# Optimization experiments

Hardware: AMD Instinct MI355X
Metric: run time of the kernel (lower is better)

## Reference

```python
import jax, jax.numpy as jnp
import numpy as np

L, B, T, C, H, V = 4, 4, 1024, 1024, 16, 32000
DH = C // H
FF = 4 * C
IGNORE = 5
EPS = 1e-5


def setup_inputs() -> dict:
    key = jax.random.key(0)
    ks = jax.random.split(key, 12)
    s = 0.02
    return {
        "idx": jax.random.randint(ks[0], (B, T), 0, V),
        "targets": jax.random.randint(ks[1], (B, T), 0, V),
        "tok_emb": jax.random.normal(ks[2], (V, C), jnp.float32) * s,
        "pos_emb": jax.random.normal(ks[3], (T, C), jnp.float32) * s,
        "Wq": jax.random.normal(ks[4], (L, C, C), jnp.float32) * s,
        "Wk": jax.random.normal(ks[5], (L, C, C), jnp.float32) * s,
        "Wv": jax.random.normal(ks[6], (L, C, C), jnp.float32) * s,
        "Wo": jax.random.normal(ks[7], (L, C, C), jnp.float32) * s,
        "bo": jnp.zeros((L, C), jnp.float32),
        "ln1_g": jnp.ones((L, C), jnp.float32),
        "ln1_b": jnp.zeros((L, C), jnp.float32),
        "ln2_g": jnp.ones((L, C), jnp.float32),
        "ln2_b": jnp.zeros((L, C), jnp.float32),
        "W1": jax.random.normal(ks[8], (L, C, FF), jnp.float32) * s,
        "b1": jnp.zeros((L, FF), jnp.float32),
        "W2": jax.random.normal(ks[9], (L, FF, C), jnp.float32) * s,
        "b2": jnp.zeros((L, C), jnp.float32),
        "lnf_g": jnp.ones((C,), jnp.float32),
        "lnf_b": jnp.zeros((C,), jnp.float32),
        "Whead": jax.random.normal(ks[10], (C, V), jnp.float32) * s,
        "bhead": jnp.zeros((V,), jnp.float32),
    }


def _layernorm(x, g, b):
    mu = jnp.mean(x, axis=-1, keepdims=True)
    var = jnp.var(x, axis=-1, keepdims=True)
    return (x - mu) * jax.lax.rsqrt(var + EPS) * g + b


def _gpt_forward(idx, targets, tok_emb, pos_emb, Wq, Wk, Wv, Wo, bo,
                 ln1_g, ln1_b, ln2_g, ln2_b, W1, b1, W2, b2,
                 lnf_g, lnf_b, Whead, bhead):
    x = tok_emb[idx] + pos_emb[None, :, :]  # [B,T,C]
    causal = jnp.tril(jnp.ones((T, T), bool))
    for i in range(L):
        h = _layernorm(x, ln1_g[i], ln1_b[i])
        q = (h @ Wq[i]).reshape(B, T, H, DH)
        k = (h @ Wk[i]).reshape(B, T, H, DH)
        v = (h @ Wv[i]).reshape(B, T, H, DH)
        wei = jnp.einsum("bqhd,bkhd->bhqk", q, k) * (DH ** -0.5)
        wei = jnp.where(causal[None, None], wei, -jnp.inf)
        wei = jax.nn.softmax(wei, axis=-1)
        att = jnp.einsum("bhqk,bkhd->bqhd", wei, v).reshape(B, T, C)
        x = x + att @ Wo[i] + bo[i]
        h = _layernorm(x, ln2_g[i], ln2_b[i])
        x = x + jax.nn.gelu(h @ W1[i] + b1[i], approximate=False) @ W2[i] + b2[i]
    x = _layernorm(x, lnf_g, lnf_b)
    logits = x @ Whead + bhead  # [B,T,V]
    # cross-entropy with ignore_index=5
    lg = logits.reshape(B * T, V)
    tg = targets.reshape(B * T)
    logp = jax.nn.log_softmax(lg, axis=-1)
    nll = -jnp.take_along_axis(logp, tg[:, None], axis=-1)[:, 0]
    valid = (tg != IGNORE).astype(lg.dtype)
    loss = jnp.sum(nll * valid) / jnp.maximum(jnp.sum(valid), 1.0)
    return logits, loss


def reference(idx, targets, tok_emb, pos_emb, Wq, Wk, Wv, Wo, bo,
              ln1_g, ln1_b, ln2_g, ln2_b, W1, b1, W2, b2,
              lnf_g, lnf_b, Whead, bhead):
    return _gpt_forward(idx, targets, tok_emb, pos_emb, Wq, Wk, Wv, Wo, bo,
                        ln1_g, ln1_b, ln2_g, ln2_b, W1, b1, W2, b2,
                        lnf_g, lnf_b, Whead, bhead)
```

## Files before the change

kernel.cpp:

```cpp
#include <hip/hip_runtime.h>
#include <cstdint>
#include <cstddef>

#define Lx 4
#define Bx 4
#define Tx 1024
#define Cx 1024
#define Hx 16
#define DHx 64
#define FFx 4096
#define Vx 32000
#define BTx 4096

typedef __attribute__((ext_vector_type(8))) __bf16 bf16x8;
typedef __attribute__((ext_vector_type(4))) float f32x4;
typedef __attribute__((ext_vector_type(8))) short short8;

__device__ __forceinline__ float bflo(unsigned u){ return __builtin_bit_cast(float, u << 16); }
__device__ __forceinline__ float bfhi(unsigned u){ return __builtin_bit_cast(float, u & 0xffff0000u); }
__device__ __forceinline__ float bf2f(short s){ return bflo((unsigned)(unsigned short)s); }
__device__ __forceinline__ short f2bf(float f){
  unsigned u = __builtin_bit_cast(unsigned, f);
  u += 0x7fffu + ((u >> 16) & 1u);
  return (short)(u >> 16);
}

__device__ __forceinline__ void gload_lds16(const short* g, short* l){
  __builtin_amdgcn_global_load_lds(
      (const __attribute__((address_space(1))) unsigned int*)g,
      (__attribute__((address_space(3))) unsigned int*)l, 16, 0, 0);
}

__device__ __forceinline__ int xcd_swizzle(int orig, int nwg){
  const int q = nwg >> 3, r = nwg & 7;
  const int xcd = orig & 7, wg = orig >> 3;
  const int base = (xcd < r) ? xcd * (q + 1) : r * (q + 1) + (xcd - r) * q;
  return base + wg;
}

__global__ __launch_bounds__(256) void embed_kernel(
    const int* __restrict__ idx, const float* __restrict__ tok,
    const float* __restrict__ pos, float* __restrict__ x)
{
  const int bt = blockIdx.x;
  const int t  = bt & (Tx - 1);
  const int tid = threadIdx.x;
  const int tk = idx[bt];
  float4 a = *(const float4*)&tok[((size_t)tk << 10) + (tid << 2)];
  const float4 p = *(const float4*)&pos[((size_t)t << 10) + (tid << 2)];
  a.x += p.x; a.y += p.y; a.z += p.z; a.w += p.w;
  *(float4*)&x[((size_t)bt << 10) + (tid << 2)] = a;
}

__global__ __launch_bounds__(256) void ln_kernel(
    const float* __restrict__ x, const float* __restrict__ g,
    const float* __restrict__ b, short* __restrict__ out)
{
  const int row = blockIdx.x;
  const int tid = threadIdx.x;
  const float4 v = *(const float4*)&x[((size_t)row << 10) + (tid << 2)];
  float s  = v.x + v.y + v.z + v.w;
  float ss = v.x*v.x + v.y*v.y + v.z*v.z + v.w*v.w;
  #pragma unroll
  for (int off = 32; off >= 1; off >>= 1) {
    s  += __shfl_down(s, off);
    ss += __shfl_down(ss, off);
  }
  __shared__ float rs[4], rss[4];
  const int lane = tid & 63, w = tid >> 6;
  if (lane == 0) { rs[w] = s; rss[w] = ss; }
  __syncthreads();
  s  = rs[0] + rs[1] + rs[2] + rs[3];
  ss = rss[0] + rss[1] + rss[2] + rss[3];
  const float mu  = s * (1.0f / Cx);
  const float var = ss * (1.0f / Cx) - mu * mu;
  const float rstd = rsqrtf(var + 1e-5f);
  const float4 g4 = *(const float4*)&g[tid << 2];
  const float4 b4 = *(const float4*)&b[tid << 2];
  short4 o;
  o.x = f2bf((v.x - mu) * rstd * g4.x + b4.x);
  o.y = f2bf((v.y - mu) * rstd * g4.y + b4.y);
  o.z = f2bf((v.z - mu) * rstd * g4.z + b4.z);
  o.w = f2bf((v.w - mu) * rstd * g4.w + b4.w);
  *(short4*)&out[((size_t)row << 10) + (tid << 2)] = o;
}

__global__ __launch_bounds__(256) void wconv_kernel(
    const float* __restrict__ W, short* __restrict__ Wt, int K, int N)
{
  __shared__ float tile[32][33];
  const int n0 = blockIdx.x << 5, k0 = blockIdx.y << 5;
  const int tx = threadIdx.x & 31, ty = threadIdx.x >> 5;
  #pragma unroll
  for (int r = 0; r < 4; ++r)
    tile[ty + (r << 3)][tx] = __builtin_nontemporal_load(
        &W[(size_t)(k0 + ty + (r << 3)) * N + n0 + tx]);
  __syncthreads();
  #pragma unroll
  for (int r = 0; r < 4; ++r)
    Wt[(size_t)(n0 + ty + (r << 3)) * K + k0 + tx] = f2bf(tile[tx][ty + (r << 3)]);
}

__global__ __launch_bounds__(256) void wconv4_kernel(
    const float* __restrict__ Wq, const float* __restrict__ Wk,
    const float* __restrict__ Wv, const float* __restrict__ Wo,
    short* __restrict__ qkvT, short* __restrict__ woT)
{
  __shared__ float tile[32][33];
  const int z = blockIdx.z;
  const float* W = (z == 0) ? Wq : (z == 1) ? Wk : (z == 2) ? Wv : Wo;
  short* Wt = (z < 3) ? qkvT + (size_t)z * Cx * Cx : woT;
  const int n0 = blockIdx.x << 5, k0 = blockIdx.y << 5;
  const int tx = threadIdx.x & 31, ty = threadIdx.x >> 5;
  #pragma unroll
  for (int r = 0; r < 4; ++r)
    tile[ty + (r << 3)][tx] = __builtin_nontemporal_load(
        &W[(size_t)(k0 + ty + (r << 3)) * Cx + n0 + tx]);
  __syncthreads();
  #pragma unroll
  for (int r = 0; r < 4; ++r)
    Wt[(size_t)(n0 + ty + (r << 3)) * Cx + k0 + tx] = f2bf(tile[tx][ty + (r << 3)]);
}

template<int MODE>
__global__ __launch_bounds__(256) void gemm_kernel(
    const short* __restrict__ A, const short* __restrict__ Bt,
    const float* __restrict__ bias, const float* __restrict__ res,
    float* __restrict__ outF, short* __restrict__ outB, int N, int K)
{
  __shared__ __align__(16) short sA[128 * 32];
  __shared__ __align__(16) short sB[128 * 32];
  const int tid  = threadIdx.x;
  const int lane = tid & 63;
  const int wave = tid >> 6;
  const int bid  = xcd_swizzle((int)blockIdx.x, (int)gridDim.x);
  const int tm = (bid & 31) << 7;
  const int tn = (bid >> 5) << 7;
  const int wm = ((wave >> 1) & 1) << 6;
  const int wn = (wave & 1) << 6;

  f32x4 acc[4][4] = {};

  const int o1  = tid << 4;
  const int row = o1 >> 6;
  const int col = (o1 & 63) >> 1;
  const short* gA1 = A  + (size_t)(tm + row) * K + col;
  const short* gA2 = A  + (size_t)(tm + row + 64) * K + col;
  const short* gB1 = Bt + (size_t)(tn + row) * K + col;
  const short* gB2 = Bt + (size_t)(tn + row + 64) * K + col;
  short* lA1 = sA + (wave << 9);
  short* lA2 = sA + 2048 + (wave << 9);
  short* lB1 = sB + (wave << 9);
  short* lB2 = sB + 2048 + (wave << 9);

  for (int k0 = 0; k0 < K; k0 += 32) {
    gload_lds16(gA1 + k0, lA1);
    gload_lds16(gA2 + k0, lA2);
    gload_lds16(gB1 + k0, lB1);
    gload_lds16(gB2 + k0, lB2);
    __syncthreads();
    bf16x8 aF[4], bF[4];
    const int kb = (lane >> 4) << 3;
    const int rsel = lane & 15;
    #pragma unroll
    for (int m = 0; m < 4; ++m)
      aF[m] = *(const bf16x8*)&sA[(wm + m * 16 + rsel) * 32 + kb];
    #pragma unroll
    for (int n = 0; n < 4; ++n)
      bF[n] = *(const bf16x8*)&sB[(wn + n * 16 + rsel) * 32 + kb];
    #pragma unroll
    for (int m = 0; m < 4; ++m) {
      #pragma unroll
      for (int n = 0; n < 4; ++n)
        acc[m][n] = __builtin_amdgcn_mfma_f32_16x16x32_bf16(aF[m], bF[n], acc[m][n], 0, 0, 0);
    }
    __syncthreads();
  }

  const int r0 = (lane >> 4) << 2;
  const int c0 = lane & 15;
  #pragma unroll
  for (int m = 0; m < 4; ++m) {
    #pragma unroll
    for (int n = 0; n < 4; ++n) {
      #pragma unroll
      for (int r = 0; r < 4; ++r) {
        const int grow = tm + wm + m * 16 + r0 + r;
        const int gcol = tn + wn + n * 16 + c0;
        const float v = acc[m][n][r];
        if constexpr (MODE == 0) {
          const int which = gcol >> 10;
          const int cc = gcol & 1023;
          const int b = grow >> 10, t = grow & 1023;
          const int hh = cc >> 6, d = cc & 63;
          outB[(size_t)which * (BTx * Cx) +
               ((size_t)((((b << 4) + hh) << 10) + t) << 6) + d] = f2bf(v);
        } else {
          const size_t o = (size_t)grow * N + gcol;
          outF[o] = res[o] + v + bias[gcol];
        }
      }
    }
  }
}

#define GBAR() do { __builtin_amdgcn_sched_barrier(0); __builtin_amdgcn_s_barrier(); __builtin_amdgcn_sched_barrier(0); } while(0)
#define VM4 asm volatile("s_waitcnt vmcnt(4)" ::: "memory");
#define NOWAIT

#define PHASE(qq, dd, STAGES, ENDW) do { \
  aF[0][0] = RD_A(dd, qq, 0, 0); aF[0][1] = RD_A(dd, qq, 0, 1); \
  aF[1][0] = RD_A(dd, qq, 1, 0); aF[1][1] = RD_A(dd, qq, 1, 1); \
  STAGES \
  GBAR(); \
  asm volatile("s_waitcnt lgkmcnt(0)" ::: "memory"); \
  __builtin_amdgcn_sched_barrier(0); \
  __builtin_amdgcn_s_setprio(1); \
  _Pragma("unroll") \
  for (int ks = 0; ks < 2; ++ks) { \
    _Pragma("unroll") \
    for (int mf = 0; mf < 2; ++mf) { \
      _Pragma("unroll") \
      for (int nf = 0; nf < 4; ++nf) \
        acc[((qq) << 1) + mf][nf] = __builtin_amdgcn_mfma_f32_16x16x32_bf16( \
            aF[mf][ks], bF[nf][ks], acc[((qq) << 1) + mf][nf], 0, 0, 0); \
    } \
  } \
  __builtin_amdgcn_s_setprio(0); \
  ENDW \
  GBAR(); \
} while (0)

#define BLOAD(dd) do { \
  _Pragma("unroll") \
  for (int nf = 0; nf < 4; ++nf) { bF[nf][0] = RD_B(dd, nf, 0); bF[nf][1] = RD_B(dd, nf, 1); } \
} while (0)

template<int MODE>
__global__ __launch_bounds__(512, 2) void gemm256_kernel(
    const short* __restrict__ A, const short* __restrict__ Bt,
    const float* __restrict__ bias, float* __restrict__ outF,
    short* __restrict__ outB, float* __restrict__ cep, int N, int K)
{
  __shared__ __align__(16) char lds[131072];
  const int tid  = threadIdx.x;
  const int lane = tid & 63;
  const int wid  = tid >> 6;
  const int wm   = wid >> 2;
  const int wn   = wid & 3;
  const int r15  = lane & 15;
  const int g4   = lane >> 4;
  const int bid  = xcd_swizzle((int)blockIdx.x, (int)gridDim.x);
  const int tm   = (bid & 15) << 8;
  const int tn   = (bid >> 4) << 8;
  const int NT   = K >> 6;
  const int NI   = NT >> 1;

  const int row0   = tid >> 3;
  const int innerE = ((tid & 7) ^ ((tid >> 3) & 7)) << 3;
  const int X0     = tid << 4;
  const short* srcA = A  + (size_t)(tm + row0) * K + innerE;
  const short* srcB = Bt + (size_t)(tn + row0) * K + innerE;
  const size_t h128K = (size_t)128 * K;
  const size_t r64K  = (size_t)64 * K;

  auto STAGE_A = [&](int t, int hh) {
    const short* s = srcA + (size_t)hh * h128K + (t << 6);
    char* d = lds + ((t & 1) << 15) + (hh << 14) + X0;
    gload_lds16(s, (short*)d);
    gload_lds16(s + r64K, (short*)(d + 8192));
  };
  auto STAGE_B = [&](int t, int hh) {
    const short* s = srcB + (size_t)hh * h128K + (t << 6);
    char* d = lds + 65536 + ((t & 1) << 15) + (hh << 14) + X0;
    gload_lds16(s, (short*)d);
    gload_lds16(s + r64K, (short*)(d + 8192));
  };

  const int arowb = (wm << 7) + r15;
  const int bcolb = (wn << 6) + r15;
  const int kchnk = g4 << 4;
  auto RD_A = [&](int d, int q, int mf, int ks) -> bf16x8 {
    const int row = arowb + (q << 5) + (mf << 4);
    return *(const bf16x8*)(lds + (d << 15) + (row << 7) +
                            ((((ks) << 6) + kchnk) ^ ((row & 7) << 4)));
  };
  auto RD_B = [&](int d, int nf, int ks) -> bf16x8 {
    const int colc = bcolb + (nf << 4);
    return *(const bf16x8*)(lds + 65536 + (d << 15) + (colc << 7) +
                            ((((ks) << 6) + kchnk) ^ ((colc & 7) << 4)));
  };

  f32x4 acc[8][4] = {};

  STAGE_A(0, 0); STAGE_A(0, 1); STAGE_B(0, 0); STAGE_B(0, 1);
  STAGE_B(1, 0); STAGE_B(1, 1);
  VM4
  GBAR();

  for (int i = 0; i < NI; ++i) {
    const int t1 = 2 * i + 1;
    const int ta = (2 * i + 2 < NT) ? 2 * i + 2 : NT - 2;
    const int tb = (2 * i + 3 < NT) ? 2 * i + 3 : NT - 1;
    bf16x8 aF[2][2], bF[4][2];
    BLOAD(0);
    PHASE(0, 0, { STAGE_A(t1, 0); },                  NOWAIT);
    PHASE(1, 0, { STAGE_A(t1, 1); STAGE_B(ta, 0); },  NOWAIT);
    PHASE(2, 0, { STAGE_B(ta, 1); },                  NOWAIT);
    PHASE(3, 0, { },                                  VM4);
    BLOAD(1);
    PHASE(0, 1, { STAGE_A(ta, 0); },                  NOWAIT);
    PHASE(1, 1, { STAGE_A(ta, 1); STAGE_B(tb, 0); },  NOWAIT);
    PHASE(2, 1, { STAGE_B(tb, 1); },                  NOWAIT);
    PHASE(3, 1, { },                                  VM4);
  }

  if constexpr (MODE == 3) {
    const int nb = tn >> 8;
    float bb4[4];
    #pragma unroll
    for (int nf = 0; nf < 4; ++nf) bb4[nf] = bias[tn + (wn << 6) + (nf << 4) + r15];
    #pragma unroll
    for (int m8 = 0; m8 < 8; ++m8)
      #pragma unroll
      for (int nf = 0; nf < 4; ++nf)
        #pragma unroll
        for (int r = 0; r < 4; ++r) acc[m8][nf][r] += bb4[nf];

    float* cepart = (float*)lds;
    #pragma unroll
    for (int m8 = 0; m8 < 8; ++m8) {
      #pragma unroll
      for (int r = 0; r < 4; ++r) {
        float sm = __expf(acc[m8][0][r]) + __expf(acc[m8][1][r])
                 + __expf(acc[m8][2][r]) + __expf(acc[m8][3][r]);
        sm += __shfl_xor(sm, 1);
        sm += __shfl_xor(sm, 2);
        sm += __shfl_xor(sm, 4);
        sm += __shfl_xor(sm, 8);
        if (r15 == 0)
          cepart[(wn << 8) + (wm << 7) + (m8 << 4) + (g4 << 2) + r] = sm;
      }
    }
    __syncthreads();
    if (tid < 256) {
      const float S = cepart[tid] + cepart[256 + tid] + cepart[512 + tid] + cepart[768 + tid];
      cep[(size_t)(tm + tid) * 125 + nb] = S;
    }

    #pragma unroll
    for (int m8 = 0; m8 < 8; ++m8) {
      #pragma unroll
      for (int nf = 0; nf < 4; ++nf) {
        #pragma unroll
        for (int r = 0; r < 4; ++r) {
          const int grow = tm + (wm << 7) + (m8 << 4) + (g4 << 2) + r;
          const int gcol = tn + (wn << 6) + (nf << 4) + r15;
          outF[(size_t)grow * N + gcol] = acc[m8][nf][r];
        }
      }
    }
  } else {
    #pragma unroll
    for (int m8 = 0; m8 < 8; ++m8) {
      #pragma unroll
      for (int nf = 0; nf < 4; ++nf) {
        #pragma unroll
        for (int r = 0; r < 4; ++r) {
          const int grow = tm + (wm << 7) + (m8 << 4) + (g4 << 2) + r;
          const int gcol = tn + (wn << 6) + (nf << 4) + r15;
          const float v = acc[m8][nf][r];
          const float t2 = v + bias[gcol];
          const float gl = 0.5f * t2 * (1.0f + erff(t2 * 0.7071067811865475f));
          outB[(size_t)grow * N + gcol] = f2bf(gl);
        }
      }
    }
  }
}

__global__ __launch_bounds__(256) void fattn_kernel(
    const short* __restrict__ q, const short* __restrict__ k,
    const short* __restrict__ v, short* __restrict__ att)
{
  __shared__ __align__(16) short sQ[4096];
  __shared__ __align__(16) short sK[4096];
  __shared__ __align__(16) short sVT[4096];
  __shared__ __align__(16) short sP[4][1024];

  const int tid  = threadIdx.x;
  const int lane = tid & 63;
  const int w    = tid >> 6;
  const int r15  = lane & 15;
  const int g4   = lane >> 4;
  const int bid  = xcd_swizzle((int)blockIdx.x, (int)gridDim.x);
  const int qt   = bid & 15;
  const int bh   = bid >> 4;

  const char* Qb = (const char*)(q + ((size_t)bh << 16)) + ((size_t)qt << 13);
  const char* Kb = (const char*)(k + ((size_t)bh << 16));
  const char* Vb = (const char*)(v + ((size_t)bh << 16));

  const int X0  = tid << 4;
  const int X1  = X0 + 4096;
  const int sw0 = X0 ^ (((X0 >> 7) & 7) << 4);
  const int sw1 = X1 ^ (((X1 >> 7) & 7) << 4);
  const int ldsOff0 = (w << 10);
  const int ldsOff1 = (w << 10) + 4096;

  gload_lds16((const short*)(Qb + sw0), (short*)((char*)sQ + ldsOff0));
  gload_lds16((const short*)(Qb + sw1), (short*)((char*)sQ + ldsOff1));
  __syncthreads();
  bf16x8 aQ[2];
  {
    const int qrow = (w << 4) + r15;
    const int base = qrow * 128 + (g4 << 4);
    const int sz = (qrow & 7) << 4;
    aQ[0] = *(const bf16x8*)((char*)sQ + ((base     ) ^ sz));
    aQ[1] = *(const bf16x8*)((char*)sQ + ((base + 64) ^ sz));
  }

  const int vdh  = (lane & 31) << 1;
  const int vkv0 = (((w << 1) + (lane >> 5)) << 3);
  const int vb0  = (vdh * 128 + vkv0 * 2)       ^ ((vdh & 7) << 4);
  const int vb1  = ((vdh + 1) * 128 + vkv0 * 2) ^ (((vdh + 1) & 7) << 4);

  float m[4] = {-3e38f, -3e38f, -3e38f, -3e38f};
  float l[4] = {0.f, 0.f, 0.f, 0.f};
  f32x4 acc_o[4] = {};
  const int qrow_g0 = (qt << 6) + (w << 4) + (g4 << 2);

  for (int kt = 0; kt <= qt; ++kt) {
    __syncthreads();
    const char* Kt = Kb + ((size_t)kt << 13);
    gload_lds16((const short*)(Kt + sw0), (short*)((char*)sK + ldsOff0));
    gload_lds16((const short*)(Kt + sw1), (short*)((char*)sK + ldsOff1));
    {
      const char* Vt = Vb + ((size_t)kt << 13);
      unsigned uv[8];
      #pragma unroll
      for (int j = 0; j < 8; ++j)
        uv[j] = *(const unsigned*)(Vt + ((vkv0 + j) << 7) + (vdh << 1));
      short8 plo, phi;
      #pragma unroll
      for (int j = 0; j < 8; ++j) {
        plo[j] = (short)(uv[j] & 0xffffu);
        phi[j] = (short)(uv[j] >> 16);
      }
      *(short8*)((char*)sVT + vb0) = plo;
      *(short8*)((char*)sVT + vb1) = phi;
    }
    __syncthreads();

    f32x4 s[4] = {};
    #pragma unroll
    for (int f = 0; f < 4; ++f) {
      const int kv = (f << 4) + r15;
      const int kb = kv * 128 + (g4 << 4);
      const int sz = (kv & 7) << 4;
      const bf16x8 b0 = *(const bf16x8*)((char*)sK + ((kb     ) ^ sz));
      const bf16x8 b1 = *(const bf16x8*)((char*)sK + ((kb + 64) ^ sz));
      s[f] = __builtin_amdgcn_mfma_f32_16x16x32_bf16(aQ[0], b0, s[f], 0, 0, 0);
      s[f] = __builtin_amdgcn_mfma_f32_16x16x32_bf16(aQ[1], b1, s[f], 0, 0, 0);
    }
    #pragma unroll
    for (int f = 0; f < 4; ++f) {
      #pragma unroll
      for (int r = 0; r < 4; ++r) {
        float sv = s[f][r] * 0.125f;
        if ((kt << 6) + (f << 4) + r15 > qrow_g0 + r) sv = -3e38f;
        s[f][r] = sv;
      }
    }
    #pragma unroll
    for (int r = 0; r < 4; ++r) {
      float mx = fmaxf(fmaxf(s[0][r], s[1][r]), fmaxf(s[2][r], s[3][r]));
      mx = fmaxf(mx, __shfl_xor(mx, 1));
      mx = fmaxf(mx, __shfl_xor(mx, 2));
      mx = fmaxf(mx, __shfl_xor(mx, 4));
      mx = fmaxf(mx, __shfl_xor(mx, 8));
      const float mn = fmaxf(m[r], mx);
      const float e  = __expf(m[r] - mn);
      float sum = 0.f;
      #pragma unroll
      for (int f = 0; f < 4; ++f) {
        const float p = __expf(s[f][r] - mn);
        s[f][r] = p; sum += p;
      }
      sum += __shfl_xor(sum, 1);
      sum += __shfl_xor(sum, 2);
      sum += __shfl_xor(sum, 4);
      sum += __shfl_xor(sum, 8);
      l[r] = l[r] * e + sum;
      m[r] = mn;
      acc_o[0][r] *= e; acc_o[1][r] *= e; acc_o[2][r] *= e; acc_o[3][r] *= e;
    }
    short* Pw = sP[w];
    #pragma unroll
    for (int f = 0; f < 4; ++f) {
      #pragma unroll
      for (int r = 0; r < 4; ++r) {
        const int prow = (g4 << 2) + r;
        const int byte = prow * 128 + (((f << 4) + r15) << 1);
        *(short*)((char*)Pw + (byte ^ ((prow & 7) << 4))) = f2bf(s[f][r]);
      }
    }
    #pragma unroll
    for (int ks = 0; ks < 2; ++ks) {
      const int ab = r15 * 128 + (ks << 6) + (g4 << 4);
      const bf16x8 aP = *(const bf16x8*)((char*)Pw + (ab ^ ((r15 & 7) << 4)));
      #pragma unroll
      for (int f = 0; f < 4; ++f) {
        const int dh = (f << 4) + r15;
        const int bb = dh * 128 + (ks << 6) + (g4 << 4);
        const bf16x8 bV = *(const bf16x8*)((char*)sVT + (bb ^ ((dh & 7) << 4)));
        acc_o[f] = __builtin_amdgcn_mfma_f32_16x16x32_bf16(aP, bV, acc_o[f], 0, 0, 0);
      }
    }
  }

  const int b = bh >> 4, hh = bh & 15;
  #pragma unroll
  for (int f = 0; f < 4; ++f) {
    #pragma unroll
    for (int r = 0; r < 4; ++r) {
      const int qg = qrow_g0 + r;
      const int dh = (f << 4) + r15;
      att[((size_t)((b << 10) + qg) << 10) + (hh << 6) + dh] = f2bf(acc_o[f][r] / l[r]);
    }
  }
}

__global__ __launch_bounds__(256) void ce_lse_kernel(
    const float* __restrict__ part, const float* __restrict__ logits,
    const int* __restrict__ tgt, float2* __restrict__ nll)
{
  const int row  = blockIdx.x * 4 + (threadIdx.x >> 6);
  const int lane = threadIdx.x & 63;
  float S = 0.f;
  #pragma unroll
  for (int p = 0; p < 2; ++p) {
    const int i = lane + (p << 6);
    if (i < 125) S += part[(size_t)row * 125 + i];
  }
  #pragma unroll
  for (int off = 32; off >= 1; off >>= 1) S += __shfl_xor(S, off);
  if (lane == 0) {
    const int tg = tgt[row];
    float v = 0.f, cnt = 0.f;
    if (tg != 5) {
      const float lt = logits[(size_t)row * Vx + tg];
      v = -(lt - logf(S));
      cnt = 1.f;
    }
    float2 o2; o2.x = v; o2.y = cnt;
    nll[row] = o2;
  }
}

__global__ __launch_bounds__(256) void ce_sum_kernel(
    const float2* __restrict__ nll, float* __restrict__ out)
{
  const int tid = threadIdx.x;
  float s = 0.f, c = 0.f;
  #pragma unroll
  for (int i = 0; i < 16; ++i) {
    const float2 v = nll[tid * 16 + i];
    s += v.x; c += v.y;
  }
  __shared__ float ls[256], lc[256];
  ls[tid] = s; lc[tid] = c;
  __syncthreads();
  for (int off = 128; off >= 1; off >>= 1) {
    if (tid < off) { ls[tid] += ls[tid + off]; lc[tid] += lc[tid + off]; }
    __syncthreads();
  }
  if (tid == 0) out[131072000ull] = ls[0] / fmaxf(lc[0], 1.0f);
}

extern "C" void kernel_launch(void* const* d_in, const int* in_sizes, int n_in,
                              void* d_out, int out_size, void* d_ws, size_t ws_size,
                              hipStream_t stream)
{
  const int*   idx     = (const int*)d_in[0];
  const int*   targets = (const int*)d_in[1];
  const float* tok_emb = (const float*)d_in[2];
  const float* pos_emb = (const float*)d_in[3];
  const float* Wq      = (const float*)d_in[4];
  const float* Wk      = (const float*)d_in[5];
  const float* Wv      = (const float*)d_in[6];
  const float* Wo      = (const float*)d_in[7];
  const float* bo      = (const float*)d_in[8];
  const float* ln1_g   = (const float*)d_in[9];
  const float* ln1_b   = (const float*)d_in[10];
  const float* ln2_g   = (const float*)d_in[11];
  const float* ln2_b   = (const float*)d_in[12];
  const float* W1      = (const float*)d_in[13];
  const float* b1      = (const float*)d_in[14];
  const float* W2      = (const float*)d_in[15];
  const float* b2      = (const float*)d_in[16];
  const float* lnf_g   = (const float*)d_in[17];
  const float* lnf_b   = (const float*)d_in[18];
  const float* Whead   = (const float*)d_in[19];
  const float* bhead   = (const float*)d_in[20];
  float* out = (float*)d_out;

  char* ws = (char*)d_ws;
  size_t off = 0;
  auto alloc = [&](size_t bytes) -> char* {
    char* p = ws + off;
    off += (bytes + 255) & ~(size_t)255;
    return p;
  };
  float* x    = (float*)alloc((size_t)BTx * Cx * 4);
  short* h    = (short*)alloc((size_t)BTx * Cx * 2);
  char*  blk  = ws + off;
  short* qb   = (short*)alloc((size_t)BTx * Cx * 2);
  short* kb   = (short*)alloc((size_t)BTx * Cx * 2);
  short* vb   = (short*)alloc((size_t)BTx * Cx * 2);
  short* attb = (short*)alloc((size_t)BTx * Cx * 2);
  short* ffb  = (short*)alloc((size_t)BTx * FFx * 2);
  short* wheadT = (short*)blk;
  short* wqkvT = (short*)alloc((size_t)3 * Cx * Cx * 2);
  short* woT  = (short*)alloc((size_t)Cx * Cx * 2);
  short* w1T  = (short*)alloc((size_t)Cx * FFx * 2);
  short* w2T  = (short*)alloc((size_t)FFx * Cx * 2);
  if (ws_size < off) return;
  float* part  = (float*)wqkvT;
  float2* nllb = (float2*)woT;

  embed_kernel<<<BTx, 256, 0, stream>>>(idx, tok_emb, pos_emb, x);

  for (int i = 0; i < Lx; ++i) {
    const size_t wo_off = (size_t)i * Cx * Cx;
    const size_t w1_off = (size_t)i * Cx * FFx;
    wconv4_kernel<<<dim3(Cx / 32, Cx / 32, 4), 256, 0, stream>>>(
        Wq + wo_off, Wk + wo_off, Wv + wo_off, Wo + wo_off, wqkvT, woT);
    wconv_kernel<<<dim3(FFx / 32, Cx / 32), 256, 0, stream>>>(W1 + w1_off, w1T, Cx, FFx);
    wconv_kernel<<<dim3(Cx / 32, FFx / 32), 256, 0, stream>>>(W2 + w1_off, w2T, FFx, Cx);

    ln_kernel<<<BTx, 256, 0, stream>>>(x, ln1_g + i * Cx, ln1_b + i * Cx, h);
    gemm_kernel<0><<<32 * 24, 256, 0, stream>>>(h, wqkvT, nullptr, nullptr, nullptr, qb, 3 * Cx, Cx);
    fattn_kernel<<<Bx * Hx * (Tx / 64), 256, 0, stream>>>(qb, kb, vb, attb);
    gemm_kernel<1><<<32 * 8, 256, 0, stream>>>(attb, woT, bo + i * Cx, x, x, nullptr, Cx, Cx);

    ln_kernel<<<BTx, 256, 0, stream>>>(x, ln2_g + i * Cx, ln2_b + i * Cx, h);
    gemm256_kernel<2><<<16 * 16, 512, 0, stream>>>(h, w1T, b1 + i * FFx, nullptr, ffb, nullptr, FFx, Cx);
    gemm_kernel<1><<<32 * 8, 256, 0, stream>>>(ffb, w2T, b2 + i * Cx, x, x, nullptr, Cx, FFx);
  }

  ln_kernel<<<BTx, 256, 0, stream>>>(x, lnf_g, lnf_b, h);
  wconv_kernel<<<dim3(Vx / 32, Cx / 32), 256, 0, stream>>>(Whead, wheadT, Cx, Vx);
  gemm256_kernel<3><<<16 * 125, 512, 0, stream>>>(h, wheadT, bhead, out, nullptr, part, Vx, Cx);

  ce_lse_kernel<<<BTx / 4, 256, 0, stream>>>(part, out, targets, nllb);
  ce_sum_kernel<<<1, 256, 0, stream>>>(nllb, out);
}
```

Before: 1.596 ms.

## Double-buffer K/V tiles in flash attention and reorder GEMM epilogue stores

The flash attention kernel now double-buffers the K and transposed V tiles in LDS. The next tile's K async copy and V global loads are issued before the current tile's compute, and V is written to the other buffer afterward, leaving one barrier per iteration. This is meant to hide global-load latency behind the MFMA work, at the cost of extra LDS and register pressure, which could lower occupancy. The GEMM epilogue also stores logits before the LSE reduction and hoists the bias load in the GELU path.

```diff
diff --git a/kernel.cpp b/kernel.cpp
--- a/kernel.cpp
+++ b/kernel.cpp
@@ -327,6 +327,19 @@
         #pragma unroll
         for (int r = 0; r < 4; ++r) acc[m8][nf][r] += bb4[nf];
 
+    #pragma unroll
+    for (int m8 = 0; m8 < 8; ++m8) {
+      #pragma unroll
+      for (int nf = 0; nf < 4; ++nf) {
+        #pragma unroll
+        for (int r = 0; r < 4; ++r) {
+          const int grow = tm + (wm << 7) + (m8 << 4) + (g4 << 2) + r;
+          const int gcol = tn + (wn << 6) + (nf << 4) + r15;
+          outF[(size_t)grow * N + gcol] = acc[m8][nf][r];
+        }
+      }
+    }
+
     float* cepart = (float*)lds;
     #pragma unroll
     for (int m8 = 0; m8 < 8; ++m8) {
@@ -347,7 +360,10 @@
       const float S = cepart[tid] + cepart[256 + tid] + cepart[512 + tid] + cepart[768 + tid];
       cep[(size_t)(tm + tid) * 125 + nb] = S;
     }
-
+  } else {
+    float bb4[4];
+    #pragma unroll
+    for (int nf = 0; nf < 4; ++nf) bb4[nf] = bias[tn + (wn << 6) + (nf << 4) + r15];
     #pragma unroll
     for (int m8 = 0; m8 < 8; ++m8) {
       #pragma unroll
@@ -356,21 +372,7 @@
         for (int r = 0; r < 4; ++r) {
           const int grow = tm + (wm << 7) + (m8 << 4) + (g4 << 2) + r;
           const int gcol = tn + (wn << 6) + (nf << 4) + r15;
-          outF[(size_t)grow * N + gcol] = acc[m8][nf][r];
-        }
-      }
-    }
-  } else {
-    #pragma unroll
-    for (int m8 = 0; m8 < 8; ++m8) {
-      #pragma unroll
-      for (int nf = 0; nf < 4; ++nf) {
-        #pragma unroll
-        for (int r = 0; r < 4; ++r) {
-          const int grow = tm + (wm << 7) + (m8 << 4) + (g4 << 2) + r;
-          const int gcol = tn + (wn << 6) + (nf << 4) + r15;
-          const float v = acc[m8][nf][r];
-          const float t2 = v + bias[gcol];
+          const float t2 = acc[m8][nf][r] + bb4[nf];
           const float gl = 0.5f * t2 * (1.0f + erff(t2 * 0.7071067811865475f));
           outB[(size_t)grow * N + gcol] = f2bf(gl);
         }
@@ -384,8 +386,8 @@
     const short* __restrict__ v, short* __restrict__ att)
 {
   __shared__ __align__(16) short sQ[4096];
-  __shared__ __align__(16) short sK[4096];
-  __shared__ __align__(16) short sVT[4096];
+  __shared__ __align__(16) short sK[2][4096];
+  __shared__ __align__(16) short sVT[2][4096];
   __shared__ __align__(16) short sP[4][1024];
 
   const int tid  = threadIdx.x;
@@ -408,9 +410,43 @@
   const int ldsOff0 = (w << 10);
   const int ldsOff1 = (w << 10) + 4096;
 
+  const int vdh  = (lane & 31) << 1;
+  const int vkv0 = (((w << 1) + (lane >> 5)) << 3);
+  const int vb0  = (vdh * 128 + vkv0 * 2)       ^ ((vdh & 7) << 4);
+  const int vb1  = ((vdh + 1) * 128 + vkv0 * 2) ^ (((vdh + 1) & 7) << 4);
+
+  auto loadV = [&](int kt, unsigned* uv) {
+    const char* Vt = Vb + ((size_t)kt << 13);
+    #pragma unroll
+    for (int j = 0; j < 8; ++j)
+      uv[j] = *(const unsigned*)(Vt + ((vkv0 + j) << 7) + (vdh << 1));
+  };
+  auto writeV = [&](int buf, const unsigned* uv) {
+    short8 plo, phi;
+    #pragma unroll
+    for (int j = 0; j < 8; ++j) {
+      plo[j] = (short)(uv[j] & 0xffffu);
+      phi[j] = (short)(uv[j] >> 16);
+    }
+    *(short8*)((char*)sVT[buf] + vb0) = plo;
+    *(short8*)((char*)sVT[buf] + vb1) = phi;
+  };
+  auto stageK = [&](int kt, int buf) {
+    const char* Kt = Kb + ((size_t)kt << 13);
+    gload_lds16((const short*)(Kt + sw0), (short*)((char*)sK[buf] + ldsOff0));
+    gload_lds16((const short*)(Kt + sw1), (short*)((char*)sK[buf] + ldsOff1));
+  };
+
   gload_lds16((const short*)(Qb + sw0), (short*)((char*)sQ + ldsOff0));
   gload_lds16((const short*)(Qb + sw1), (short*)((char*)sQ + ldsOff1));
+  stageK(0, 0);
+  {
+    unsigned uv[8];
+    loadV(0, uv);
+    writeV(0, uv);
+  }
   __syncthreads();
+
   bf16x8 aQ[2];
   {
     const int qrow = (w << 4) + r15;
@@ -420,37 +456,18 @@
     aQ[1] = *(const bf16x8*)((char*)sQ + ((base + 64) ^ sz));
   }
 
-  const int vdh  = (lane & 31) << 1;
-  const int vkv0 = (((w << 1) + (lane >> 5)) << 3);
-  const int vb0  = (vdh * 128 + vkv0 * 2)       ^ ((vdh & 7) << 4);
-  const int vb1  = ((vdh + 1) * 128 + vkv0 * 2) ^ (((vdh + 1) & 7) << 4);
-
   float m[4] = {-3e38f, -3e38f, -3e38f, -3e38f};
   float l[4] = {0.f, 0.f, 0.f, 0.f};
   f32x4 acc_o[4] = {};
   const int qrow_g0 = (qt << 6) + (w << 4) + (g4 << 2);
 
   for (int kt = 0; kt <= qt; ++kt) {
-    __syncthreads();
-    const char* Kt = Kb + ((size_t)kt << 13);
-    gload_lds16((const short*)(Kt + sw0), (short*)((char*)sK + ldsOff0));
-    gload_lds16((const short*)(Kt + sw1), (short*)((char*)sK + ldsOff1));
-    {
-      const char* Vt = Vb + ((size_t)kt << 13);
-      unsigned uv[8];
-      #pragma unroll
-      for (int j = 0; j < 8; ++j)
-        uv[j] = *(const unsigned*)(Vt + ((vkv0 + j) << 7) + (vdh << 1));
-      short8 plo, phi;
-      #pragma unroll
-      for (int j = 0; j < 8; ++j) {
-        plo[j] = (short)(uv[j] & 0xffffu);
-        phi[j] = (short)(uv[j] >> 16);
-      }
-      *(short8*)((char*)sVT + vb0) = plo;
-      *(short8*)((char*)sVT + vb1) = phi;
-    }
-    __syncthreads();
+    const int cur = kt & 1;
+    unsigned uv2[8];
+    if (kt < qt) {
+      stageK(kt + 1, cur ^ 1);
+      loadV(kt + 1, uv2);
+    }
 
     f32x4 s[4] = {};
     #pragma unroll
@@ -458,8 +475,8 @@
       const int kv = (f << 4) + r15;
       const int kb = kv * 128 + (g4 << 4);
       const int sz = (kv & 7) << 4;
-      const bf16x8 b0 = *(const bf16x8*)((char*)sK + ((kb     ) ^ sz));
-      const bf16x8 b1 = *(const bf16x8*)((char*)sK + ((kb + 64) ^ sz));
+      const bf16x8 b0 = *(const bf16x8*)((char*)sK[cur] + ((kb     ) ^ sz));
+      const bf16x8 b1 = *(const bf16x8*)((char*)sK[cur] + ((kb + 64) ^ sz));
       s[f] = __builtin_amdgcn_mfma_f32_16x16x32_bf16(aQ[0], b0, s[f], 0, 0, 0);
       s[f] = __builtin_amdgcn_mfma_f32_16x16x32_bf16(aQ[1], b1, s[f], 0, 0, 0);
     }
@@ -513,10 +530,13 @@
       for (int f = 0; f < 4; ++f) {
         const int dh = (f << 4) + r15;
         const int bb = dh * 128 + (ks << 6) + (g4 << 4);
-        const bf16x8 bV = *(const bf16x8*)((char*)sVT + (bb ^ ((dh & 7) << 4)));
+        const bf16x8 bV = *(const bf16x8*)((char*)sVT[cur] + (bb ^ ((dh & 7) << 4)));
         acc_o[f] = __builtin_amdgcn_mfma_f32_16x16x32_bf16(aP, bV, acc_o[f], 0, 0, 0);
       }
     }
+
+    if (kt < qt) writeV(cur ^ 1, uv2);
+    __syncthreads();
   }
 
   const int b = bh >> 4, hh = bh & 15;
```

Measured after the change: 1.541 ms. -3.4%, faster.
